# Kernel tuning notes

Measured on AMD Instinct MI355X. Metric: run time of the kernel, lower is better.

Reference implementation:

```python
import jax, jax.numpy as jnp
import numpy as np

DIM = 1024
HEADS = 16
GROUPS = 4
DIM_HEAD = 64
INNER = HEADS * DIM_HEAD  # 1024
KV_DIM = 2 * DIM_HEAD * GROUPS  # 512
B, N = 4, 2048
EPS = 1e-6


def _layernorm(x, scale, bias, eps=EPS):
    mu = jnp.mean(x, axis=-1, keepdims=True)
    var = jnp.mean(jnp.square(x - mu), axis=-1, keepdims=True)
    return (x - mu) * jax.lax.rsqrt(var + eps) * scale + bias


def setup_inputs() -> dict:
    key = jax.random.key(0)
    ks = jax.random.split(key, 10)
    lecun = lambda k, shape: jax.random.normal(k, shape, jnp.float32) * (1.0 / np.sqrt(shape[0]))
    return {
        "x": jax.random.normal(ks[0], (B, N, DIM), jnp.float32),
        "ln_scale": jnp.ones((DIM,), jnp.float32),
        "ln_bias": jnp.zeros((DIM,), jnp.float32),
        "Wq": lecun(ks[1], (DIM, INNER)),
        "Wkv": lecun(ks[2], (DIM, KV_DIM)),
        "qn_scale": jnp.ones((DIM_HEAD,), jnp.float32),
        "qn_bias": jnp.zeros((DIM_HEAD,), jnp.float32),
        "kn_scale": jnp.ones((DIM_HEAD,), jnp.float32),
        "kn_bias": jnp.zeros((DIM_HEAD,), jnp.float32),
        "Wout": lecun(ks[3], (INNER, DIM)),
    }


def reference(x, ln_scale, ln_bias, Wq, Wkv, qn_scale, qn_bias, kn_scale, kn_bias, Wout):
    b, n, _ = x.shape
    g, hg, d = GROUPS, HEADS // GROUPS, DIM_HEAD
    scale = d ** -0.5
    xn = _layernorm(x, ln_scale, ln_bias)
    # q: (b,n,inner) -> (b,h,n,d)
    q = (xn @ Wq).reshape(b, n, HEADS, d).transpose(0, 2, 1, 3)
    kv = xn @ Wkv
    k, v = jnp.split(kv, 2, axis=-1)
    # (b,n,g*d) -> (b,g,n,d)
    k = k.reshape(b, n, g, d).transpose(0, 2, 1, 3)
    v = v.reshape(b, n, g, d).transpose(0, 2, 1, 3)
    q = _layernorm(q, qn_scale, qn_bias)
    k = _layernorm(k, kn_scale, kn_bias)
    # split heads into groups: (b, g*hg, n, d) -> (b, g, hg, n, d)
    qg = q.reshape(b, g, hg, n, d)
    dots = jnp.einsum('bghqd,bgkd->bghqk', qg, k) * scale
    attn = jax.nn.softmax(dots, axis=-1)
    out = jnp.einsum('bghqk,bgkd->bghqd', attn, v)  # (b,g,hg,n,d)
    out = out.transpose(0, 3, 1, 2, 4).reshape(b, n, g * hg * d)
    return out @ Wout
```

## Files before the change

kernel.cpp:

```cpp
#include <hip/hip_runtime.h>
#include <cstdint>
#include <cstddef>

typedef unsigned short u16;
typedef __attribute__((ext_vector_type(4))) float f32x4;
typedef __attribute__((ext_vector_type(8))) __bf16 bf16x8;
typedef __attribute__((ext_vector_type(4))) __bf16 bf16x4;
typedef __attribute__((ext_vector_type(8))) unsigned short u16x8;
typedef __attribute__((ext_vector_type(4))) unsigned short u16x4;

#define DEV static __device__ __forceinline__

#if __has_builtin(__builtin_amdgcn_exp2f)
#define EXP2(x) __builtin_amdgcn_exp2f(x)
#else
#define EXP2(x) exp2f(x)
#endif

DEV float bf2f(u16 v) { return __uint_as_float(((unsigned)v) << 16); }
DEV u16 f2bf(float f) {
  unsigned u = __float_as_uint(f);
  return (u16)((u + 0x7FFFu + ((u >> 16) & 1u)) >> 16);
}

DEV void gl_lds16(const void* g, void* l) {
  __builtin_amdgcn_global_load_lds((const __attribute__((address_space(1))) void*)g,
                                   (__attribute__((address_space(3))) void*)l, 16, 0, 0);
}

__global__ __launch_bounds__(256) void transpose64(const float* __restrict__ in,
                                                   u16* __restrict__ out, int incols) {
  __shared__ __attribute__((aligned(16))) u16 t[64 * 72];
  const int r0 = blockIdx.x * 64, c0 = blockIdx.y * 64, tid = threadIdx.x;
#pragma unroll
  for (int i = 0; i < 2; i++) {
    int c = i * 256 + tid;
    int row = c >> 3, cc = c & 7;
    const float* src = &in[(size_t)(r0 + row) * incols + c0 + cc * 8];
    f32x4 v0 = *(const f32x4*)src;
    f32x4 v1 = *(const f32x4*)(src + 4);
    u16x8 o;
#pragma unroll
    for (int j = 0; j < 4; j++) { o[j] = f2bf(v0[j]); o[4 + j] = f2bf(v1[j]); }
    *(u16x8*)&t[row * 72 + cc * 8] = o;
  }
  __syncthreads();
#pragma unroll
  for (int i = 0; i < 2; i++) {
    int c = i * 256 + tid;
    int d = c >> 3, nc = c & 7;
    u16x8 o;
#pragma unroll
    for (int j = 0; j < 8; j++) o[j] = t[(nc * 8 + j) * 72 + d];
    *(u16x8*)&out[(size_t)(c0 + d) * 1024 + r0 + nc * 8] = o;
  }
}

__global__ __launch_bounds__(256) void ln_x(const float* __restrict__ x,
                                            const float* __restrict__ sc,
                                            const float* __restrict__ bi,
                                            u16* __restrict__ xn) {
  __shared__ float red[8];
  const int row = blockIdx.x, tid = threadIdx.x;
  const int w = tid >> 6;
  f32x4 f = *(const f32x4*)&x[(size_t)row * 1024 + tid * 4];
  float s = f[0] + f[1] + f[2] + f[3];
  float q = f[0] * f[0] + f[1] * f[1] + f[2] * f[2] + f[3] * f[3];
#pragma unroll
  for (int off = 1; off < 64; off <<= 1) {
    s += __shfl_xor(s, off);
    q += __shfl_xor(q, off);
  }
  if ((tid & 63) == 0) { red[w] = s; red[4 + w] = q; }
  __syncthreads();
  float S = red[0] + red[1] + red[2] + red[3];
  float Q = red[4] + red[5] + red[6] + red[7];
  float mu = S * (1.0f / 1024.0f);
  float var = Q * (1.0f / 1024.0f) - mu * mu;
  float rs = rsqrtf(var + 1e-6f);
  f32x4 scv = *(const f32x4*)&sc[tid * 4];
  f32x4 biv = *(const f32x4*)&bi[tid * 4];
  u16* o = xn + (size_t)row * 1024 + tid * 4;
#pragma unroll
  for (int j = 0; j < 4; j++) o[j] = f2bf((f[j] - mu) * rs * scv[j] + biv[j]);
}

template <bool F32OUT>
__global__ __launch_bounds__(256) void gemm_bt(const u16* __restrict__ A,
                                               const u16* __restrict__ Bt,
                                               void* __restrict__ Cp,
                                               int M, int N, int K) {
  __shared__ __attribute__((aligned(16))) u16 Als[128 * 64];
  __shared__ __attribute__((aligned(16))) u16 Bls[128 * 64];
  const int tid = threadIdx.x;
  const int w = tid >> 6, lane = tid & 63, ln = lane & 15, quad = lane >> 4;
  const int m0 = blockIdx.y * 128, n0 = blockIdx.x * 128;
  const int moff = (w & 1) * 64, noff = (w >> 1) * 64;
  const f32x4 fzero = {0.f, 0.f, 0.f, 0.f};
  f32x4 acc[4][4];
#pragma unroll
  for (int i = 0; i < 4; i++)
#pragma unroll
    for (int j = 0; j < 4; j++) acc[i][j] = fzero;

  const u16* aS[4];
  const u16* bS[4];
#pragma unroll
  for (int i = 0; i < 4; i++) {
    int s = i * 256 + tid;
    int row = s >> 3, cs = (s & 7) ^ (row & 7);
    aS[i] = A + (size_t)(m0 + row) * K + cs * 8;
    bS[i] = Bt + (size_t)(n0 + row) * K + cs * 8;
  }

  for (int k0 = 0; k0 < K; k0 += 64) {
    __syncthreads();
#pragma unroll
    for (int i = 0; i < 4; i++) {
      int s = i * 256 + tid;
      gl_lds16(aS[i] + k0, &Als[s * 8]);
      gl_lds16(bS[i] + k0, &Bls[s * 8]);
    }
    __syncthreads();
#pragma unroll
    for (int kk = 0; kk < 2; kk++) {
      bf16x8 af[4], bfv[4];
#pragma unroll
      for (int mi = 0; mi < 4; mi++)
        af[mi] = *(const bf16x8*)
            &Als[(moff + mi * 16 + ln) * 64 + (((kk * 4 + quad) ^ (ln & 7)) * 8)];
#pragma unroll
      for (int ni = 0; ni < 4; ni++)
        bfv[ni] = *(const bf16x8*)
            &Bls[(noff + ni * 16 + ln) * 64 + (((kk * 4 + quad) ^ (ln & 7)) * 8)];
#pragma unroll
      for (int mi = 0; mi < 4; mi++)
#pragma unroll
        for (int ni = 0; ni < 4; ni++)
          acc[mi][ni] = __builtin_amdgcn_mfma_f32_16x16x32_bf16(af[mi], bfv[ni],
                                                                acc[mi][ni], 0, 0, 0);
    }
  }
#pragma unroll
  for (int mi = 0; mi < 4; mi++)
#pragma unroll
    for (int ni = 0; ni < 4; ni++)
#pragma unroll
      for (int r = 0; r < 4; r++) {
        size_t m = m0 + moff + mi * 16 + quad * 4 + r;
        size_t n = n0 + noff + ni * 16 + ln;
        if (F32OUT)
          ((float*)Cp)[m * N + n] = acc[mi][ni][r];
        else
          ((u16*)Cp)[m * N + n] = f2bf(acc[mi][ni][r]);
      }
}

__global__ __launch_bounds__(256) void gemm_qkv(const u16* __restrict__ A,
                                                const u16* __restrict__ Bt,
                                                const float* __restrict__ qs,
                                                const float* __restrict__ qb,
                                                const float* __restrict__ ks,
                                                const float* __restrict__ kb,
                                                u16* __restrict__ Qout,
                                                u16* __restrict__ Kout,
                                                u16* __restrict__ Vraw) {
  const int M = 8192, N = 1536, K = 1024;
  (void)M; (void)N;
  __shared__ __attribute__((aligned(16))) u16 Als[128 * 64];
  __shared__ __attribute__((aligned(16))) u16 Bls[128 * 64];
  const int tid = threadIdx.x;
  const int w = tid >> 6, lane = tid & 63, ln = lane & 15, quad = lane >> 4;
  const int m0 = blockIdx.y * 128, n0 = blockIdx.x * 128;
  const int moff = (w & 1) * 64, noff = (w >> 1) * 64;
  const f32x4 fzero = {0.f, 0.f, 0.f, 0.f};
  f32x4 acc[4][4];
#pragma unroll
  for (int i = 0; i < 4; i++)
#pragma unroll
    for (int j = 0; j < 4; j++) acc[i][j] = fzero;

  const u16* aS[4];
  const u16* bS[4];
#pragma unroll
  for (int i = 0; i < 4; i++) {
    int s = i * 256 + tid;
    int row = s >> 3, cs = (s & 7) ^ (row & 7);
    aS[i] = A + (size_t)(m0 + row) * K + cs * 8;
    bS[i] = Bt + (size_t)(n0 + row) * K + cs * 8;
  }

  for (int k0 = 0; k0 < K; k0 += 64) {
    __syncthreads();
#pragma unroll
    for (int i = 0; i < 4; i++) {
      int s = i * 256 + tid;
      gl_lds16(aS[i] + k0, &Als[s * 8]);
      gl_lds16(bS[i] + k0, &Bls[s * 8]);
    }
    __syncthreads();
#pragma unroll
    for (int kk = 0; kk < 2; kk++) {
      bf16x8 af[4], bfv[4];
#pragma unroll
      for (int mi = 0; mi < 4; mi++)
        af[mi] = *(const bf16x8*)
            &Als[(moff + mi * 16 + ln) * 64 + (((kk * 4 + quad) ^ (ln & 7)) * 8)];
#pragma unroll
      for (int ni = 0; ni < 4; ni++)
        bfv[ni] = *(const bf16x8*)
            &Bls[(noff + ni * 16 + ln) * 64 + (((kk * 4 + quad) ^ (ln & 7)) * 8)];
#pragma unroll
      for (int mi = 0; mi < 4; mi++)
#pragma unroll
        for (int ni = 0; ni < 4; ni++)
          acc[mi][ni] = __builtin_amdgcn_mfma_f32_16x16x32_bf16(af[mi], bfv[ni],
                                                                acc[mi][ni], 0, 0, 0);
    }
  }

  const int nb = n0 + noff;
  if (nb < 1280) {
    const float SCL = 0.18033688011112042f;
    const bool isQ = (nb < 1024);
    const float* scp = isQ ? qs : ks;
    const float* bip = isQ ? qb : kb;
    const float mul = isQ ? SCL : 1.0f;
    float scl[4], bia[4];
#pragma unroll
    for (int ni = 0; ni < 4; ni++) {
      scl[ni] = scp[ni * 16 + ln];
      bia[ni] = bip[ni * 16 + ln];
    }
#pragma unroll
    for (int mi = 0; mi < 4; mi++)
#pragma unroll
      for (int r = 0; r < 4; r++) {
        const int m = m0 + moff + mi * 16 + quad * 4 + r;
        const int bidx = m >> 11, nseq = m & 2047;
        float v0 = acc[mi][0][r], v1 = acc[mi][1][r];
        float v2 = acc[mi][2][r], v3 = acc[mi][3][r];
        float s = (v0 + v1) + (v2 + v3);
        float q2 = (v0 * v0 + v1 * v1) + (v2 * v2 + v3 * v3);
#pragma unroll
        for (int off = 1; off < 16; off <<= 1) {
          s += __shfl_xor(s, off);
          q2 += __shfl_xor(q2, off);
        }
        const float mu = s * (1.0f / 64.0f);
        const float var = q2 * (1.0f / 64.0f) - mu * mu;
        const float rs = rsqrtf(var + 1e-6f);
        u16* op;
        if (isQ) {
          const int h = nb >> 6;
          op = Qout + ((size_t)(bidx * 16 + h) * 2048 + nseq) * 64;
        } else {
          const int g = (nb - 1024) >> 6;
          op = Kout + ((size_t)(bidx * 4 + g) * 2048 + nseq) * 64;
        }
        op[0 * 16 + ln] = f2bf(((v0 - mu) * rs * scl[0] + bia[0]) * mul);
        op[1 * 16 + ln] = f2bf(((v1 - mu) * rs * scl[1] + bia[1]) * mul);
        op[2 * 16 + ln] = f2bf(((v2 - mu) * rs * scl[2] + bia[2]) * mul);
        op[3 * 16 + ln] = f2bf(((v3 - mu) * rs * scl[3] + bia[3]) * mul);
      }
  } else {
    const int g2 = nb - 1280;
#pragma unroll
    for (int mi = 0; mi < 4; mi++)
#pragma unroll
      for (int r = 0; r < 4; r++) {
        const int m = m0 + moff + mi * 16 + quad * 4 + r;
        u16* op = Vraw + (size_t)m * 256 + g2;
#pragma unroll
        for (int ni = 0; ni < 4; ni++) op[ni * 16 + ln] = f2bf(acc[mi][ni][r]);
      }
  }
}

__global__ __launch_bounds__(256) void vtrans(const u16* __restrict__ Vraw,
                                              u16* __restrict__ Vt) {
  __shared__ __attribute__((aligned(16))) u16 t[64 * 72];
  const int n0 = blockIdx.x * 64;
  const int bg = blockIdx.y;
  const int b = bg >> 2, g = bg & 3;
  const int tid = threadIdx.x;
  const u16* src = Vraw + (size_t)(b * 2048 + n0) * 256 + g * 64;
#pragma unroll
  for (int i = 0; i < 2; i++) {
    int c = i * 256 + tid;
    int row = c >> 3, cc = c & 7;
    *(f32x4*)&t[row * 72 + cc * 8] = *(const f32x4*)&src[(size_t)row * 256 + cc * 8];
  }
  __syncthreads();
  u16* dst = Vt + (size_t)bg * 64 * 2048 + n0;
#pragma unroll
  for (int i = 0; i < 2; i++) {
    int c = i * 256 + tid;
    int d = c >> 3, nc = c & 7;
    const int pA = 32 * (nc >> 2) + (nc & 1) * 16 + ((nc >> 1) & 1) * 4;
    u16x8 o;
#pragma unroll
    for (int j = 0; j < 8; j++) o[j] = t[(nc * 8 + j) * 72 + d];
    u16x4 lo = {o[0], o[1], o[2], o[3]};
    u16x4 hi = {o[4], o[5], o[6], o[7]};
    *(u16x4*)&dst[(size_t)d * 2048 + pA] = lo;
    *(u16x4*)&dst[(size_t)d * 2048 + pA + 8] = hi;
  }
}

__global__ __launch_bounds__(128, 2) void attn(const u16* __restrict__ Q,
                                               const u16* __restrict__ Kb,
                                               const u16* __restrict__ Vt,
                                               u16* __restrict__ Out) {
  __shared__ __attribute__((aligned(16))) u16 Kls0[64 * 64];
  __shared__ __attribute__((aligned(16))) u16 Kls1[64 * 64];
  __shared__ __attribute__((aligned(16))) u16 Vls0[64 * 64];
  __shared__ __attribute__((aligned(16))) u16 Vls1[64 * 64];
  const int qt = blockIdx.x;
  const int bh = blockIdx.y;
  const int b = bh >> 4, h = bh & 15, g = h >> 2;
  const int tid = threadIdx.x, w = tid >> 6, lane = tid & 63;
  const int ln = lane & 15, quad = lane >> 4;
  const u16* Qg = Q + ((size_t)(b * 16 + h) * 2048 + qt * 128 + w * 64) * 64;
  const u16* Kg = Kb + (size_t)(b * 4 + g) * 2048 * 64;
  const u16* Vg = Vt + (size_t)(b * 4 + g) * 64 * 2048;
  const f32x4 fzero = {0.f, 0.f, 0.f, 0.f};

  bf16x8 qf[4][2];
#pragma unroll
  for (int mi = 0; mi < 4; mi++)
#pragma unroll
    for (int ks2 = 0; ks2 < 2; ks2++)
      qf[mi][ks2] = *(const bf16x8*)&Qg[(size_t)(mi * 16 + ln) * 64 + ks2 * 32 + quad * 8];

  f32x4 oacc[4][4];
#pragma unroll
  for (int ni = 0; ni < 4; ni++)
#pragma unroll
    for (int mi = 0; mi < 4; mi++) oacc[ni][mi] = fzero;
  f32x4 rsum[4];
#pragma unroll
  for (int mi = 0; mi < 4; mi++) rsum[mi] = fzero;
  bf16x8 vones;
#pragma unroll
  for (int j = 0; j < 8; j++) vones[j] = (__bf16)1.0f;

  int krow[4], kcs[4];
#pragma unroll
  for (int i = 0; i < 4; i++) {
    int s = i * 128 + tid;
    krow[i] = s >> 3;
    kcs[i] = (s & 7) ^ (krow[i] & 7);
  }

  auto STAGE = [&](int kt, u16* Kd, u16* Vd) {
#pragma unroll
    for (int i = 0; i < 4; i++) {
      int s = i * 128 + tid;
      gl_lds16(Kg + (size_t)(kt * 64 + krow[i]) * 64 + kcs[i] * 8, &Kd[s * 8]);
      gl_lds16(Vg + (size_t)krow[i] * 2048 + kt * 64 + kcs[i] * 8, &Vd[s * 8]);
    }
  };

  auto BODY = [&](int kt, const u16* K_, const u16* V_, u16* Kn, u16* Vn) {
    if (kt + 1 < 32) STAGE(kt + 1, Kn, Vn);

#pragma unroll
    for (int c = 0; c < 2; c++) {
      bf16x8 kf[2][2];
#pragma unroll
      for (int ni = 0; ni < 2; ni++) {
        const int kr = (c * 32 + ni * 16 + ln) * 64;
        kf[ni][0] = *(const bf16x8*)&K_[kr + ((quad ^ (ln & 7)) * 8)];
        kf[ni][1] = *(const bf16x8*)&K_[kr + (((4 + quad) ^ (ln & 7)) * 8)];
      }

      f32x4 sacc[4][2];
      __builtin_amdgcn_s_setprio(1);
#pragma unroll
      for (int ni = 0; ni < 2; ni++)
#pragma unroll
        for (int mi = 0; mi < 4; mi++) {
          f32x4 tt = __builtin_amdgcn_mfma_f32_16x16x32_bf16(kf[ni][0], qf[mi][0],
                                                             fzero, 0, 0, 0);
          sacc[mi][ni] = __builtin_amdgcn_mfma_f32_16x16x32_bf16(kf[ni][1], qf[mi][1],
                                                                 tt, 0, 0, 0);
        }
      __builtin_amdgcn_s_setprio(0);

      bf16x8 pfa[4];
#pragma unroll
      for (int mi = 0; mi < 4; mi++) {
        pfa[mi][0] = (__bf16)EXP2(sacc[mi][0][0]);
        pfa[mi][1] = (__bf16)EXP2(sacc[mi][0][1]);
        pfa[mi][2] = (__bf16)EXP2(sacc[mi][0][2]);
        pfa[mi][3] = (__bf16)EXP2(sacc[mi][0][3]);
        pfa[mi][4] = (__bf16)EXP2(sacc[mi][1][0]);
        pfa[mi][5] = (__bf16)EXP2(sacc[mi][1][1]);
        pfa[mi][6] = (__bf16)EXP2(sacc[mi][1][2]);
        pfa[mi][7] = (__bf16)EXP2(sacc[mi][1][3]);
      }

#pragma unroll
      for (int mi = 0; mi < 4; mi++)
        rsum[mi] = __builtin_amdgcn_mfma_f32_16x16x32_bf16(vones, pfa[mi],
                                                           rsum[mi], 0, 0, 0);

#pragma unroll
      for (int ni = 0; ni < 4; ni++) {
        bf16x8 vf = *(const bf16x8*)
            &V_[(ni * 16 + ln) * 64 + (((4 * c + quad) ^ (ln & 7)) * 8)];
        __builtin_amdgcn_s_setprio(1);
#pragma unroll
        for (int mi = 0; mi < 4; mi++)
          oacc[ni][mi] = __builtin_amdgcn_mfma_f32_16x16x32_bf16(vf, pfa[mi],
                                                                 oacc[ni][mi], 0, 0, 0);
        __builtin_amdgcn_s_setprio(0);
      }
    }
    __syncthreads();
  };

  STAGE(0, Kls0, Vls0);
  __syncthreads();
  for (int kt = 0; kt < 32; kt += 2) {
    BODY(kt, Kls0, Vls0, Kls1, Vls1);
    BODY(kt + 1, Kls1, Vls1, Kls0, Vls0);
  }

#pragma unroll
  for (int mi = 0; mi < 4; mi++) {
    float inv = 1.0f / rsum[mi][0];
    u16* Og = Out + ((size_t)b * 2048 + qt * 128 + w * 64 + mi * 16 + ln) * 1024 + h * 64;
#pragma unroll
    for (int ni = 0; ni < 4; ni++) {
      bf16x4 ov = {(__bf16)(oacc[ni][mi][0] * inv), (__bf16)(oacc[ni][mi][1] * inv),
                   (__bf16)(oacc[ni][mi][2] * inv), (__bf16)(oacc[ni][mi][3] * inv)};
      *(bf16x4*)&Og[ni * 16 + quad * 4] = ov;
    }
  }
}

extern "C" void kernel_launch(void* const* d_in, const int* in_sizes, int n_in,
                              void* d_out, int out_size, void* d_ws, size_t ws_size,
                              hipStream_t stream) {
  const float* x    = (const float*)d_in[0];
  const float* lns  = (const float*)d_in[1];
  const float* lnb  = (const float*)d_in[2];
  const float* Wq   = (const float*)d_in[3];
  const float* Wkv  = (const float*)d_in[4];
  const float* qns  = (const float*)d_in[5];
  const float* qnb  = (const float*)d_in[6];
  const float* kns  = (const float*)d_in[7];
  const float* knb  = (const float*)d_in[8];
  const float* Wout = (const float*)d_in[9];
  float* out = (float*)d_out;
  char* ws = (char*)d_ws;

  const size_t o_xn = 0;
  const size_t o_q  = 16777216;
  const size_t o_vr = o_q + 16777216;
  const size_t o_bt = o_vr + 4194304;
  const size_t o_k  = o_bt + 3145728;
  const size_t o_vt = o_k + 4194304;
  u16* xn   = (u16*)(ws + o_xn);
  u16* Qbuf = (u16*)(ws + o_q);
  u16* Vraw = (u16*)(ws + o_vr);
  u16* bt   = (u16*)(ws + o_bt);
  u16* Kbuf = (u16*)(ws + o_k);
  u16* Vtb  = (u16*)(ws + o_vt);
  u16* aout = xn;

  transpose64<<<dim3(16, 16), 256, 0, stream>>>(Wq, bt, 1024);
  transpose64<<<dim3(16, 8), 256, 0, stream>>>(Wkv, bt + 1024 * 1024, 512);
  ln_x<<<8192, 256, 0, stream>>>(x, lns, lnb, xn);
  gemm_qkv<<<dim3(12, 64), 256, 0, stream>>>(xn, bt, qns, qnb, kns, knb,
                                             Qbuf, Kbuf, Vraw);
  transpose64<<<dim3(16, 16), 256, 0, stream>>>(Wout, bt, 1024);
  vtrans<<<dim3(32, 16), 256, 0, stream>>>(Vraw, Vtb);
  attn<<<dim3(16, 64), 128, 0, stream>>>(Qbuf, Kbuf, Vtb, aout);
  gemm_bt<true><<<dim3(8, 64), 256, 0, stream>>>(aout, bt, out, 8192, 1024, 1024);

  (void)in_sizes; (void)n_in; (void)out_size; (void)ws_size;
}
```

Measured before the change: 248.4 us.

## Split attention key chunks across wave pairs and reduce partials via LDS

Result: slower. 625.7 us (+151.8%).

```diff
diff --git a/kernel.cpp b/kernel.cpp
--- a/kernel.cpp
+++ b/kernel.cpp
@@ -308,20 +308,23 @@
   }
 }
 
-__global__ __launch_bounds__(128, 2) void attn(const u16* __restrict__ Q,
+__global__ __launch_bounds__(256, 4) void attn(const u16* __restrict__ Q,
                                                const u16* __restrict__ Kb,
                                                const u16* __restrict__ Vt,
                                                u16* __restrict__ Out) {
-  __shared__ __attribute__((aligned(16))) u16 Kls0[64 * 64];
-  __shared__ __attribute__((aligned(16))) u16 Kls1[64 * 64];
-  __shared__ __attribute__((aligned(16))) u16 Vls0[64 * 64];
-  __shared__ __attribute__((aligned(16))) u16 Vls1[64 * 64];
+  __shared__ __attribute__((aligned(16))) char smem[34816];
+  u16* const Kls0 = (u16*)smem;
+  u16* const Kls1 = (u16*)(smem + 8192);
+  u16* const Vls0 = (u16*)(smem + 16384);
+  u16* const Vls1 = (u16*)(smem + 24576);
   const int qt = blockIdx.x;
   const int bh = blockIdx.y;
   const int b = bh >> 4, h = bh & 15, g = h >> 2;
   const int tid = threadIdx.x, w = tid >> 6, lane = tid & 63;
   const int ln = lane & 15, quad = lane >> 4;
-  const u16* Qg = Q + ((size_t)(b * 16 + h) * 2048 + qt * 128 + w * 64) * 64;
+  const int qh = w >> 1;
+  const int kh = w & 1;
+  const u16* Qg = Q + ((size_t)(b * 16 + h) * 2048 + qt * 128 + qh * 64) * 64;
   const u16* Kg = Kb + (size_t)(b * 4 + g) * 2048 * 64;
   const u16* Vg = Vt + (size_t)(b * 4 + g) * 64 * 2048;
   const f32x4 fzero = {0.f, 0.f, 0.f, 0.f};
@@ -345,18 +348,18 @@
 #pragma unroll
   for (int j = 0; j < 8; j++) vones[j] = (__bf16)1.0f;
 
-  int krow[4], kcs[4];
-#pragma unroll
-  for (int i = 0; i < 4; i++) {
-    int s = i * 128 + tid;
+  int krow[2], kcs[2];
+#pragma unroll
+  for (int i = 0; i < 2; i++) {
+    int s = i * 256 + tid;
     krow[i] = s >> 3;
     kcs[i] = (s & 7) ^ (krow[i] & 7);
   }
 
   auto STAGE = [&](int kt, u16* Kd, u16* Vd) {
 #pragma unroll
-    for (int i = 0; i < 4; i++) {
-      int s = i * 128 + tid;
+    for (int i = 0; i < 2; i++) {
+      int s = i * 256 + tid;
       gl_lds16(Kg + (size_t)(kt * 64 + krow[i]) * 64 + kcs[i] * 8, &Kd[s * 8]);
       gl_lds16(Vg + (size_t)krow[i] * 2048 + kt * 64 + kcs[i] * 8, &Vd[s * 8]);
     }
@@ -365,58 +368,55 @@
   auto BODY = [&](int kt, const u16* K_, const u16* V_, u16* Kn, u16* Vn) {
     if (kt + 1 < 32) STAGE(kt + 1, Kn, Vn);
 
-#pragma unroll
-    for (int c = 0; c < 2; c++) {
-      bf16x8 kf[2][2];
-#pragma unroll
-      for (int ni = 0; ni < 2; ni++) {
-        const int kr = (c * 32 + ni * 16 + ln) * 64;
-        kf[ni][0] = *(const bf16x8*)&K_[kr + ((quad ^ (ln & 7)) * 8)];
-        kf[ni][1] = *(const bf16x8*)&K_[kr + (((4 + quad) ^ (ln & 7)) * 8)];
+    bf16x8 kf[2][2];
+#pragma unroll
+    for (int ni = 0; ni < 2; ni++) {
+      const int kr = (kh * 32 + ni * 16 + ln) * 64;
+      kf[ni][0] = *(const bf16x8*)&K_[kr + ((quad ^ (ln & 7)) * 8)];
+      kf[ni][1] = *(const bf16x8*)&K_[kr + (((4 + quad) ^ (ln & 7)) * 8)];
+    }
+
+    f32x4 sacc[4][2];
+    __builtin_amdgcn_s_setprio(1);
+#pragma unroll
+    for (int ni = 0; ni < 2; ni++)
+#pragma unroll
+      for (int mi = 0; mi < 4; mi++) {
+        f32x4 tt = __builtin_amdgcn_mfma_f32_16x16x32_bf16(kf[ni][0], qf[mi][0],
+                                                           fzero, 0, 0, 0);
+        sacc[mi][ni] = __builtin_amdgcn_mfma_f32_16x16x32_bf16(kf[ni][1], qf[mi][1],
+                                                               tt, 0, 0, 0);
       }
-
-      f32x4 sacc[4][2];
+    __builtin_amdgcn_s_setprio(0);
+
+    bf16x8 pfa[4];
+#pragma unroll
+    for (int mi = 0; mi < 4; mi++) {
+      pfa[mi][0] = (__bf16)EXP2(sacc[mi][0][0]);
+      pfa[mi][1] = (__bf16)EXP2(sacc[mi][0][1]);
+      pfa[mi][2] = (__bf16)EXP2(sacc[mi][0][2]);
+      pfa[mi][3] = (__bf16)EXP2(sacc[mi][0][3]);
+      pfa[mi][4] = (__bf16)EXP2(sacc[mi][1][0]);
+      pfa[mi][5] = (__bf16)EXP2(sacc[mi][1][1]);
+      pfa[mi][6] = (__bf16)EXP2(sacc[mi][1][2]);
+      pfa[mi][7] = (__bf16)EXP2(sacc[mi][1][3]);
+    }
+
+#pragma unroll
+    for (int mi = 0; mi < 4; mi++)
+      rsum[mi] = __builtin_amdgcn_mfma_f32_16x16x32_bf16(vones, pfa[mi],
+                                                         rsum[mi], 0, 0, 0);
+
+#pragma unroll
+    for (int ni = 0; ni < 4; ni++) {
+      bf16x8 vf = *(const bf16x8*)
+          &V_[(ni * 16 + ln) * 64 + (((4 * kh + quad) ^ (ln & 7)) * 8)];
       __builtin_amdgcn_s_setprio(1);
 #pragma unroll
-      for (int ni = 0; ni < 2; ni++)
-#pragma unroll
-        for (int mi = 0; mi < 4; mi++) {
-          f32x4 tt = __builtin_amdgcn_mfma_f32_16x16x32_bf16(kf[ni][0], qf[mi][0],
-                                                             fzero, 0, 0, 0);
-          sacc[mi][ni] = __builtin_amdgcn_mfma_f32_16x16x32_bf16(kf[ni][1], qf[mi][1],
-                                                                 tt, 0, 0, 0);
-        }
+      for (int mi = 0; mi < 4; mi++)
+        oacc[ni][mi] = __builtin_amdgcn_mfma_f32_16x16x32_bf16(vf, pfa[mi],
+                                                               oacc[ni][mi], 0, 0, 0);
       __builtin_amdgcn_s_setprio(0);
-
-      bf16x8 pfa[4];
-#pragma unroll
-      for (int mi = 0; mi < 4; mi++) {
-        pfa[mi][0] = (__bf16)EXP2(sacc[mi][0][0]);
-        pfa[mi][1] = (__bf16)EXP2(sacc[mi][0][1]);
-        pfa[mi][2] = (__bf16)EXP2(sacc[mi][0][2]);
-        pfa[mi][3] = (__bf16)EXP2(sacc[mi][0][3]);
-        pfa[mi][4] = (__bf16)EXP2(sacc[mi][1][0]);
-        pfa[mi][5] = (__bf16)EXP2(sacc[mi][1][1]);
-        pfa[mi][6] = (__bf16)EXP2(sacc[mi][1][2]);
-        pfa[mi][7] = (__bf16)EXP2(sacc[mi][1][3]);
-      }
-
-#pragma unroll
-      for (int mi = 0; mi < 4; mi++)
-        rsum[mi] = __builtin_amdgcn_mfma_f32_16x16x32_bf16(vones, pfa[mi],
-                                                           rsum[mi], 0, 0, 0);
-
-#pragma unroll
-      for (int ni = 0; ni < 4; ni++) {
-        bf16x8 vf = *(const bf16x8*)
-            &V_[(ni * 16 + ln) * 64 + (((4 * c + quad) ^ (ln & 7)) * 8)];
-        __builtin_amdgcn_s_setprio(1);
-#pragma unroll
-        for (int mi = 0; mi < 4; mi++)
-          oacc[ni][mi] = __builtin_amdgcn_mfma_f32_16x16x32_bf16(vf, pfa[mi],
-                                                                 oacc[ni][mi], 0, 0, 0);
-        __builtin_amdgcn_s_setprio(0);
-      }
     }
     __syncthreads();
   };
@@ -428,15 +428,35 @@
     BODY(kt + 1, Kls1, Vls1, Kls0, Vls0);
   }
 
-#pragma unroll
-  for (int mi = 0; mi < 4; mi++) {
-    float inv = 1.0f / rsum[mi][0];
-    u16* Og = Out + ((size_t)b * 2048 + qt * 128 + w * 64 + mi * 16 + ln) * 1024 + h * 64;
-#pragma unroll
-    for (int ni = 0; ni < 4; ni++) {
-      bf16x4 ov = {(__bf16)(oacc[ni][mi][0] * inv), (__bf16)(oacc[ni][mi][1] * inv),
-                   (__bf16)(oacc[ni][mi][2] * inv), (__bf16)(oacc[ni][mi][3] * inv)};
-      *(bf16x4*)&Og[ni * 16 + quad * 4] = ov;
+  float* const od = (float*)smem;
+  float* const rd = (float*)(smem + 32768);
+  if (kh == 0) {
+    float* myo = od + qh * 4096;
+#pragma unroll
+    for (int ni = 0; ni < 4; ni++)
+#pragma unroll
+      for (int mi = 0; mi < 4; mi++)
+        *(f32x4*)&myo[(ni * 4 + mi) * 256 + lane * 4] = oacc[ni][mi];
+    f32x4 rv = {rsum[0][0], rsum[1][0], rsum[2][0], rsum[3][0]};
+    *(f32x4*)&rd[qh * 256 + lane * 4] = rv;
+  }
+  __syncthreads();
+  if (kh == 1) {
+    const float* po = od + qh * 4096;
+    f32x4 rv = *(const f32x4*)&rd[qh * 256 + lane * 4];
+#pragma unroll
+    for (int mi = 0; mi < 4; mi++) {
+      float inv = 1.0f / (rsum[mi][0] + rv[mi]);
+      u16* Og = Out + ((size_t)b * 2048 + qt * 128 + qh * 64 + mi * 16 + ln) * 1024 + h * 64;
+#pragma unroll
+      for (int ni = 0; ni < 4; ni++) {
+        f32x4 p = *(const f32x4*)&po[(ni * 4 + mi) * 256 + lane * 4];
+        bf16x4 ov = {(__bf16)((oacc[ni][mi][0] + p[0]) * inv),
+                     (__bf16)((oacc[ni][mi][1] + p[1]) * inv),
+                     (__bf16)((oacc[ni][mi][2] + p[2]) * inv),
+                     (__bf16)((oacc[ni][mi][3] + p[3]) * inv)};
+        *(bf16x4*)&Og[ni * 16 + quad * 4] = ov;
+      }
     }
   }
 }
@@ -478,7 +498,7 @@
                                              Qbuf, Kbuf, Vraw);
   transpose64<<<dim3(16, 16), 256, 0, stream>>>(Wout, bt, 1024);
   vtrans<<<dim3(32, 16), 256, 0, stream>>>(Vraw, Vtb);
-  attn<<<dim3(16, 64), 128, 0, stream>>>(Qbuf, Kbuf, Vtb, aout);
+  attn<<<dim3(16, 64), 256, 0, stream>>>(Qbuf, Kbuf, Vtb, aout);
   gemm_bt<true><<<dim3(8, 64), 256, 0, stream>>>(aout, bt, out, 8192, 1024, 1024);
 
   (void)in_sizes; (void)n_in; (void)out_size; (void)ws_size;
```
